# Kernel tuning notes

Measured on AMD Instinct MI355X. Metric: run time of the kernel, lower is better.

The kernel has to match this reference:

```python
import jax, jax.numpy as jnp
import numpy as np

WS = 8  # window_size


def _lstm(x, params):
    """Multi-layer batch-first LSTM with zero initial state (PyTorch gate order i,f,g,o).
    x: [B, Tw, F] -> (outputs [B, Tw, H], (h_n [L,B,H], c_n [L,B,H]))"""
    B = x.shape[0]
    hs_final, cs_final = [], []
    inp = x
    for (Wih, Whh, bih, bhh) in params:
        H = Whh.shape[1]
        b = bih + bhh

        def step(carry, xt, Wih=Wih, Whh=Whh, b=b):
            h, c = carry
            g = xt @ Wih.T + h @ Whh.T + b          # [B, 4H]
            i, f, gg, o = jnp.split(g, 4, axis=-1)
            c = jax.nn.sigmoid(f) * c + jax.nn.sigmoid(i) * jnp.tanh(gg)
            h = jax.nn.sigmoid(o) * jnp.tanh(c)
            return (h, c), h

        h0 = jnp.zeros((B, H), x.dtype)
        (hT, cT), hs = jax.lax.scan(step, (h0, h0), jnp.swapaxes(inp, 0, 1))
        inp = jnp.swapaxes(hs, 0, 1)
        hs_final.append(hT)
        cs_final.append(cT)
    return inp, (jnp.stack(hs_final), jnp.stack(cs_final))


def setup_inputs() -> dict:
    key = jax.random.key(0)
    ks = jax.random.split(key, 11)
    B, T, H, IN = 64, 256, 64, 4
    s = 0.1
    return {
        "traj": jax.random.normal(ks[0], (B, T, IN), jnp.float32),
        "W_ih0": jax.random.normal(ks[1], (4 * H, IN), jnp.float32) * s,
        "W_hh0": jax.random.normal(ks[2], (4 * H, H), jnp.float32) * s,
        "b_ih0": jax.random.normal(ks[3], (4 * H,), jnp.float32) * s,
        "b_hh0": jax.random.normal(ks[4], (4 * H,), jnp.float32) * s,
        "W_ih1": jax.random.normal(ks[5], (4 * H, H), jnp.float32) * s,
        "W_hh1": jax.random.normal(ks[6], (4 * H, H), jnp.float32) * s,
        "b_ih1": jax.random.normal(ks[7], (4 * H,), jnp.float32) * s,
        "b_hh1": jax.random.normal(ks[8], (4 * H,), jnp.float32) * s,
        "W_lin": jax.random.normal(ks[9], (2, H), jnp.float32) * s,
        "b_lin": jax.random.normal(ks[10], (2,), jnp.float32) * s,
    }


def reference(traj, W_ih0, W_hh0, b_ih0, b_hh0, W_ih1, W_hh1, b_ih1, b_hh1, W_lin, b_lin):
    params = [(W_ih0, W_hh0, b_ih0, b_hh0), (W_ih1, W_hh1, b_ih1, b_hh1)]
    lin = lambda x: x @ W_lin.T + b_lin
    B, T = traj.shape[0], traj.shape[1]

    # initial window: teacher-forced, residual update from true state
    lo, hidden = _lstm(traj[:, :WS, :], params)
    out = traj[:, WS - 1:WS, 2:] + lin(lo[:, -1:, :])  # [B, 1, 2]

    # warm-up loop: window mixes remaining true inputs with own predictions
    for t in range(1, WS):
        fb = jnp.concatenate(
            [traj[:, WS + t - 1:WS + t - 1 + out.shape[1], 0:2], out], axis=2)
        x = jnp.concatenate([traj[:, t:WS, :], fb], axis=1)  # [B, WS, 4]
        lo, hidden = _lstm(x, params)
        out = jnp.concatenate([out, out[:, -1:, :] + lin(lo[:, -1:, :])], axis=1)

    # main rollout: each step re-runs the LSTM on a fresh WS-window built from
    # true controls (cols 0:2) and the last WS predictions. Carry a rolling buffer.
    ctrl = traj[:, :, 0:2]

    def step2(carry, t):
        buf, hid = carry  # buf: [B, WS, 2]
        win = jax.lax.dynamic_slice(ctrl, (0, t, 0), (B, WS, 2))
        lo, hid = _lstm(jnp.concatenate([win, buf], axis=2), params)
        new = buf[:, -1:, :] + lin(lo[:, -1:, :])  # [B, 1, 2]
        buf = jnp.concatenate([buf[:, 1:, :], new], axis=1)
        return (buf, hid), new[:, 0, :]

    (buf, hidden), news = jax.lax.scan(step2, (out, hidden), jnp.arange(WS, T - WS))
    out = jnp.concatenate([out, jnp.swapaxes(news, 0, 1)], axis=1)  # [B, T-WS, 2]
    return out, hidden[0], hidden[1]
```

## Files before the change

### kernel.cpp

```cpp
#include <hip/hip_runtime.h>
#include <math.h>

typedef float4 f4;
typedef unsigned long long u64;
#define NW 248
#define NB 64
#define NPH2 (NW + 8)

__device__ __forceinline__ float tanh_f(float x) { return 2.0f * __builtin_amdgcn_rcpf(1.0f + __expf(-2.0f * x)) - 1.0f; }

template<int CTRL>
__device__ __forceinline__ float dppf(float v) {
    return __int_as_float(__builtin_amdgcn_update_dpp(0, __float_as_int(v), CTRL, 0xF, 0xF, true));
}
#define XOR1 0xB1
#define XOR2 0x4E
#define MIR7 0x141
#define BC0  0x00
#define BC1  0x55
#define BC2  0xAA
#define BC3  0xFF

#define OPQ1(X) asm volatile("" : "+v"(X));
#define OPQ4(V) OPQ1(V.x) OPQ1(V.y) OPQ1(V.z) OPQ1(V.w)

#define FMA4(acc,W,H) { acc=fmaf((W).x,(H).x,acc); acc=fmaf((W).y,(H).y,acc); \
                        acc=fmaf((W).z,(H).z,acc); acc=fmaf((W).w,(H).w,acc); }

#define TAIL8(CC, SA, SB, VA, VB, HN)                                                     \
    {                                                                                     \
        float r0=dppf<XOR1>(Q1), r1=dppf<XOR1>(Q0), r2=dppf<XOR1>(Q3), r3=dppf<XOR1>(Q2); \
        float r4=dppf<XOR1>(Q5), r5=dppf<XOR1>(Q4), r6=dppf<XOR1>(Q7), r7=dppf<XOR1>(Q6); \
        Q0+=r0; Q1+=r1; Q2+=r2; Q3+=r3; Q4+=r4; Q5+=r5; Q6+=r6; Q7+=r7;                   \
        float u0=dppf<XOR2>(Q2), u3=dppf<XOR2>(Q1), u4=dppf<XOR2>(Q6), u7=dppf<XOR2>(Q5); \
        Q0+=u0; Q3+=u3; Q4+=u4; Q7+=u7;                                                   \
        float m0=dppf<MIR7>(Q3), m4=dppf<MIR7>(Q7);                                       \
        Q0+=m0; Q4+=m4;                                                                   \
        const float yv = lolane ? Q0 : Q4;                                                \
        const float av = fmaf(fs2, __builtin_amdgcn_rcpf(1.f + __expf(kae*yv)), fs3);     \
        const float gi = dppf<BC0>(av);                                                   \
        const float gf = dppf<BC1>(av);                                                   \
        const float gg = dppf<BC2>(av);                                                   \
        const float go = dppf<BC3>(av);                                                   \
        const bool rst = lolane ? ((SA)==0) : ((SB)==0);                                  \
        const bool upd = lolane ? (VA) : (VB);                                            \
        const float igv = gi * gg;                                                        \
        const float ccn = rst ? igv : fmaf(gf, CC, igv);                                  \
        CC = upd ? ccn : CC;                                                              \
        HN = go * tanh_f(CC);                                                             \
    }

__device__ __forceinline__ float xsel4(float x0, float x1, float x2, float x3, int q2) {
    return (q2 & 2) ? ((q2 & 1) ? x3 : x2) : ((q2 & 1) ? x1 : x0);
}

__device__ __forceinline__ float xload(const float* trajS, const float (*outr)[2],
                                       int w, int s, int q2) {
    float x0, x1, x2, x3;
    if (w == 0) {
        x0 = trajS[s*4+0]; x1 = trajS[s*4+1]; x2 = trajS[s*4+2]; x3 = trajS[s*4+3];
    } else if (w < 8) {
        if (s < 8 - w) {
            const int tt = w + s;
            x0 = trajS[tt*4+0]; x1 = trajS[tt*4+1]; x2 = trajS[tt*4+2]; x3 = trajS[tt*4+3];
        } else {
            const int tc = 2*w + s - 1;
            const int jo2 = (w + s - 8) & 7;
            x0 = trajS[tc*4+0]; x1 = trajS[tc*4+1];
            x2 = outr[jo2][0];  x3 = outr[jo2][1];
        }
    } else {
        const int tc = w + s;
        const int jo2 = (w + s) & 7;
        x0 = trajS[tc*4+0]; x1 = trajS[tc*4+1];
        x2 = outr[jo2][0];  x3 = outr[jo2][1];
    }
    return xsel4(x0, x1, x2, x3, q2);
}

__global__ __launch_bounds__(512) __attribute__((amdgpu_waves_per_eu(2, 2)))
void or_lstm_coop(const float* __restrict__ traj,
                  const float* __restrict__ Wih0, const float* __restrict__ Whh0,
                  const float* __restrict__ bih0, const float* __restrict__ bhh0,
                  const float* __restrict__ Wih1, const float* __restrict__ Whh1,
                  const float* __restrict__ bih1, const float* __restrict__ bhh1,
                  const float* __restrict__ Wlin, const float* __restrict__ blin,
                  float* __restrict__ out, u64* __restrict__ ring)
{
    const int bid  = blockIdx.x;
    const int row  = bid & 63;
    const int half = bid >> 6;
    const int tid  = threadIdx.x;
    const int j    = tid >> 3;
    const int idx  = tid & 7;
    const int q2   = idx & 3;

    __shared__ __align__(16) float trajS[256 * 4];
    __shared__ __align__(16) float X0[2][4][64];
    __shared__ __align__(16) float X1[2][4][64];
    __shared__ float outr[8][2];

    if (tid < 256)
        ((f4*)trajS)[tid] = ((const f4*)(traj + (size_t)row * 256 * 4))[tid];
    ((float*)X0)[tid] = 0.f;
    ((float*)X1)[tid] = 0.f;

    const int jo = j * 64 + idx * 8;
    const int v0 = q2, v1 = 1 ^ q2, v2 = 2 ^ q2, v3 = 3 ^ q2;
    f4 W0a = *(const f4*)(Whh0 + v0*4096 + jo), W0b = *(const f4*)(Whh0 + v0*4096 + jo + 4);
    f4 W1a = *(const f4*)(Whh0 + v1*4096 + jo), W1b = *(const f4*)(Whh0 + v1*4096 + jo + 4);
    f4 W2a = *(const f4*)(Whh0 + v2*4096 + jo), W2b = *(const f4*)(Whh0 + v2*4096 + jo + 4);
    f4 W3a = *(const f4*)(Whh0 + v3*4096 + jo), W3b = *(const f4*)(Whh0 + v3*4096 + jo + 4);
    f4 U0a = *(const f4*)(Wih1 + v0*4096 + jo), U0b = *(const f4*)(Wih1 + v0*4096 + jo + 4);
    f4 U1a = *(const f4*)(Wih1 + v1*4096 + jo), U1b = *(const f4*)(Wih1 + v1*4096 + jo + 4);
    f4 U2a = *(const f4*)(Wih1 + v2*4096 + jo), U2b = *(const f4*)(Wih1 + v2*4096 + jo + 4);
    f4 U3a = *(const f4*)(Wih1 + v3*4096 + jo), U3b = *(const f4*)(Wih1 + v3*4096 + jo + 4);
    f4 V0a = *(const f4*)(Whh1 + v0*4096 + jo), V0b = *(const f4*)(Whh1 + v0*4096 + jo + 4);
    f4 V1a = *(const f4*)(Whh1 + v1*4096 + jo), V1b = *(const f4*)(Whh1 + v1*4096 + jo + 4);
    f4 V2a = *(const f4*)(Whh1 + v2*4096 + jo), V2b = *(const f4*)(Whh1 + v2*4096 + jo + 4);
    f4 V3a = *(const f4*)(Whh1 + v3*4096 + jo), V3b = *(const f4*)(Whh1 + v3*4096 + jo + 4);
    OPQ4(W0a) OPQ4(W0b) OPQ4(W1a) OPQ4(W1b) OPQ4(W2a) OPQ4(W2b) OPQ4(W3a) OPQ4(W3b)
    OPQ4(U0a) OPQ4(U0b) OPQ4(U1a) OPQ4(U1b) OPQ4(U2a) OPQ4(U2b) OPQ4(U3a) OPQ4(U3b)
    OPQ4(V0a) OPQ4(V0b) OPQ4(V1a) OPQ4(V1b) OPQ4(V2a) OPQ4(V2b) OPQ4(V3a) OPQ4(V3b)

    float wx0 = (idx < 4) ? Wih0[v0*256 + j*4 + q2] : 0.f;
    float wx1 = (idx < 4) ? Wih0[v1*256 + j*4 + q2] : 0.f;
    float wx2 = (idx < 4) ? Wih0[v2*256 + j*4 + q2] : 0.f;
    float wx3 = (idx < 4) ? Wih0[v3*256 + j*4 + q2] : 0.f;
    float bb00 = (idx == 0) ? (bih0[0*64+j] + bhh0[0*64+j]) : 0.f;
    float bb01 = (idx == 0) ? (bih0[1*64+j] + bhh0[1*64+j]) : 0.f;
    float bb02 = (idx == 0) ? (bih0[2*64+j] + bhh0[2*64+j]) : 0.f;
    float bb03 = (idx == 0) ? (bih0[3*64+j] + bhh0[3*64+j]) : 0.f;
    float bb10 = (idx == 0) ? (bih1[0*64+j] + bhh1[0*64+j]) : 0.f;
    float bb11 = (idx == 0) ? (bih1[1*64+j] + bhh1[1*64+j]) : 0.f;
    float bb12 = (idx == 0) ? (bih1[2*64+j] + bhh1[2*64+j]) : 0.f;
    float bb13 = (idx == 0) ? (bih1[3*64+j] + bhh1[3*64+j]) : 0.f;
    OPQ1(wx0) OPQ1(wx1) OPQ1(wx2) OPQ1(wx3)
    OPQ1(bb00) OPQ1(bb01) OPQ1(bb02) OPQ1(bb03)
    OPQ1(bb10) OPQ1(bb11) OPQ1(bb12) OPQ1(bb13)

    const float kae = (q2 == 2) ? -2.f : -1.f;
    const float fs2 = (q2 == 2) ?  2.f :  1.f;
    const float fs3 = (q2 == 2) ? -1.f :  0.f;

    float wl0 = 0.f, wl1 = 0.f;
    if (tid < 64) { wl0 = Wlin[tid]; wl1 = Wlin[64 + tid]; }
    const float bl0 = blin[0], bl1 = blin[1];

    const bool lolane = (idx < 4);
    float cc0[2] = {0.f, 0.f};
    float cc1[2] = {0.f, 0.f};

    __syncthreads();

    for (int p = 0; p < NPH2; ++p) {
        const int par = p & 1;
        const float* X0r = &X0[par ^ 1][0][idx * 8];
        const float* X1r = &X1[par ^ 1][0][idx * 8];
        float* X0w = &X0[par][0][j];
        float* X1w = &X1[par][0][j];

        float QM[2][8];

        #pragma unroll
        for (int P = 0; P < 2; ++P) {
            const int cA = 4*half + 2*P, cB = cA + 1;
            const int lA = 2*P,          lB = lA + 1;
            const int sA0 = (p - cA) & 7,     sB0 = (p - cB) & 7;
            const int sA1 = (p - 1 - cA) & 7, sB1 = (p - 1 - cB) & 7;
            const bool vA1 = (unsigned)(p - 1 - sA1) < (unsigned)NW;
            const bool vB1 = (unsigned)(p - 1 - sB1) < (unsigned)NW;

            const f4 ha = *(const f4*)(X0r + lA*64), hb = *(const f4*)(X0r + lA*64 + 4);
            const f4 hc = *(const f4*)(X0r + lB*64), hd = *(const f4*)(X0r + lB*64 + 4);

            {
                float qa0=bb00, qa1=bb01, qa2=bb02, qa3=bb03;
                float qb0=0.f,  qb1=0.f,  qb2=0.f,  qb3=0.f;
                float qa4=bb00, qa5=bb01, qa6=bb02, qa7=bb03;
                float qb4=0.f,  qb5=0.f,  qb6=0.f,  qb7=0.f;
                if (sA0 != 0) {
                    FMA4(qa0, W0a, ha) FMA4(qb0, W0b, hb)
                    FMA4(qa1, W1a, ha) FMA4(qb1, W1b, hb)
                    FMA4(qa2, W2a, ha) FMA4(qb2, W2b, hb)
                    FMA4(qa3, W3a, ha) FMA4(qb3, W3b, hb)
                }
                if (sB0 != 0) {
                    FMA4(qa4, W0a, hc) FMA4(qb4, W0b, hd)
                    FMA4(qa5, W1a, hc) FMA4(qb5, W1b, hd)
                    FMA4(qa6, W2a, hc) FMA4(qb6, W2b, hd)
                    FMA4(qa7, W3a, hc) FMA4(qb7, W3b, hd)
                }
                QM[P][0]=qa0+qb0; QM[P][1]=qa1+qb1; QM[P][2]=qa2+qb2; QM[P][3]=qa3+qb3;
                QM[P][4]=qa4+qb4; QM[P][5]=qa5+qb5; QM[P][6]=qa6+qb6; QM[P][7]=qa7+qb7;
            }

            {
                float pa0=bb10, pa1=bb11, pa2=bb12, pa3=bb13;
                float pb0=0.f,  pb1=0.f,  pb2=0.f,  pb3=0.f;
                float pa4=bb10, pa5=bb11, pa6=bb12, pa7=bb13;
                float pb4=0.f,  pb5=0.f,  pb6=0.f,  pb7=0.f;
                FMA4(pa0, U0a, ha) FMA4(pb0, U0b, hb)
                FMA4(pa1, U1a, ha) FMA4(pb1, U1b, hb)
                FMA4(pa2, U2a, ha) FMA4(pb2, U2b, hb)
                FMA4(pa3, U3a, ha) FMA4(pb3, U3b, hb)
                FMA4(pa4, U0a, hc) FMA4(pb4, U0b, hd)
                FMA4(pa5, U1a, hc) FMA4(pb5, U1b, hd)
                FMA4(pa6, U2a, hc) FMA4(pb6, U2b, hd)
                FMA4(pa7, U3a, hc) FMA4(pb7, U3b, hd)
                if (sA1 != 0) {
                    const f4 ea = *(const f4*)(X1r + lA*64), eb = *(const f4*)(X1r + lA*64 + 4);
                    FMA4(pa0, V0a, ea) FMA4(pb0, V0b, eb)
                    FMA4(pa1, V1a, ea) FMA4(pb1, V1b, eb)
                    FMA4(pa2, V2a, ea) FMA4(pb2, V2b, eb)
                    FMA4(pa3, V3a, ea) FMA4(pb3, V3b, eb)
                }
                if (sB1 != 0) {
                    const f4 ec = *(const f4*)(X1r + lB*64), ed = *(const f4*)(X1r + lB*64 + 4);
                    FMA4(pa4, V0a, ec) FMA4(pb4, V0b, ed)
                    FMA4(pa5, V1a, ec) FMA4(pb5, V1b, ed)
                    FMA4(pa6, V2a, ec) FMA4(pb6, V2b, ed)
                    FMA4(pa7, V3a, ec) FMA4(pb7, V3b, ed)
                }
                float Q0 = pa0+pb0, Q1 = pa1+pb1, Q2 = pa2+pb2, Q3 = pa3+pb3;
                float Q4 = pa4+pb4, Q5 = pa5+pb5, Q6 = pa6+pb6, Q7 = pa7+pb7;
                float hn1;
                TAIL8(cc1[P], sA1, sB1, vA1, vB1, hn1)
                if (vA1 && idx == 0) X1w[lA*64] = hn1;
                if (vB1 && idx == 4) X1w[lB*64] = hn1;
            }
        }
        __syncthreads();

        if (p >= 8) {
            const int w1 = p - 8;
            const int gs = p & 7;
            u64* rp = ring + ((size_t)row * 16 + (p & 15)) * 2;
            const unsigned tag = (unsigned)(p + 1);
            if ((gs >> 2) == half) {
                if (tid < 64) {
                    const float hval = X1[par][gs & 3][tid];
                    float r0 = wl0 * hval, r1 = wl1 * hval;
                    #pragma unroll
                    for (int off = 32; off > 0; off >>= 1) {
                        r0 += __shfl_down(r0, off);
                        r1 += __shfl_down(r1, off);
                    }
                    if (tid == 0) {
                        const float prev0 = w1 ? outr[(w1-1) & 7][0] : trajS[7*4+2];
                        const float prev1 = w1 ? outr[(w1-1) & 7][1] : trajS[7*4+3];
                        const float o0 = prev0 + r0 + bl0;
                        const float o1 = prev1 + r1 + bl1;
                        outr[w1 & 7][0] = o0; outr[w1 & 7][1] = o1;
                        out[((size_t)row * NW + w1) * 2 + 0] = o0;
                        out[((size_t)row * NW + w1) * 2 + 1] = o1;
                        const u64 pk0 = ((u64)tag << 32) | (u64)__float_as_uint(o0);
                        const u64 pk1 = ((u64)tag << 32) | (u64)__float_as_uint(o1);
                        __hip_atomic_store(&rp[0], pk0, __ATOMIC_RELEASE, __HIP_MEMORY_SCOPE_AGENT);
                        __hip_atomic_store(&rp[1], pk1, __ATOMIC_RELEASE, __HIP_MEMORY_SCOPE_AGENT);
                    }
                }
            } else {
                if (tid == 0) {
                    u64 va, vb;
                    do { va = __hip_atomic_load(&rp[0], __ATOMIC_ACQUIRE, __HIP_MEMORY_SCOPE_AGENT);
                    } while ((unsigned)(va >> 32) != tag);
                    do { vb = __hip_atomic_load(&rp[1], __ATOMIC_ACQUIRE, __HIP_MEMORY_SCOPE_AGENT);
                    } while ((unsigned)(vb >> 32) != tag);
                    outr[w1 & 7][0] = __uint_as_float((unsigned)va);
                    outr[w1 & 7][1] = __uint_as_float((unsigned)vb);
                }
            }
        }
        __syncthreads();

        float xs0, xs1, xs2, xs3;
        if (p >= 15) {
            const float xc = xsel4(trajS[p*4+0], trajS[p*4+1],
                                   outr[p & 7][0], outr[p & 7][1], q2);
            xs0 = xs1 = xs2 = xs3 = xc;
        } else {
            float t[4];
            #pragma unroll
            for (int c = 0; c < 4; ++c) {
                const int g = 4*half + c;
                const int s = (p - g) & 7;
                const int w = p - s;
                t[c] = ((unsigned)w < (unsigned)NW) ? xload(trajS, outr, w, s, q2) : 0.f;
            }
            xs0 = t[0]; xs1 = t[1]; xs2 = t[2]; xs3 = t[3];
        }
        #pragma unroll
        for (int P = 0; P < 2; ++P) {
            const int cA = 4*half + 2*P, cB = cA + 1;
            const int lA = 2*P,          lB = lA + 1;
            const int sA0 = (p - cA) & 7, sB0 = (p - cB) & 7;
            const bool vA0 = (unsigned)(p - sA0) < (unsigned)NW;
            const bool vB0 = (unsigned)(p - sB0) < (unsigned)NW;
            const float xA = P ? xs2 : xs0;
            const float xB = P ? xs3 : xs1;
            float Q0 = fmaf(wx0, xA, QM[P][0]);
            float Q1 = fmaf(wx1, xA, QM[P][1]);
            float Q2 = fmaf(wx2, xA, QM[P][2]);
            float Q3 = fmaf(wx3, xA, QM[P][3]);
            float Q4 = fmaf(wx0, xB, QM[P][4]);
            float Q5 = fmaf(wx1, xB, QM[P][5]);
            float Q6 = fmaf(wx2, xB, QM[P][6]);
            float Q7 = fmaf(wx3, xB, QM[P][7]);
            float hn0;
            TAIL8(cc0[P], sA0, sB0, vA0, vB0, hn0)
            if (vA0 && idx == 0) X0w[lA*64] = hn0;
            if (vB0 && idx == 4) X0w[lB*64] = hn0;
        }
        __syncthreads();
    }

    if (half == 1 && idx == 4) {
        float* hn = out + (size_t)NB * NW * 2;
        float* cn = hn + 2 * NB * 64;
        hn[(0 * NB + row) * 64 + j] = X0[0][3][j];
        hn[(1 * NB + row) * 64 + j] = X1[1][3][j];
        cn[(0 * NB + row) * 64 + j] = cc0[1];
        cn[(1 * NB + row) * 64 + j] = cc1[1];
    }
}

extern "C" void kernel_launch(void* const* d_in, const int* in_sizes, int n_in,
                              void* d_out, int out_size, void* d_ws, size_t ws_size,
                              hipStream_t stream) {
    const float* traj = (const float*)d_in[0];
    const float* Wih0 = (const float*)d_in[1];
    const float* Whh0 = (const float*)d_in[2];
    const float* bih0 = (const float*)d_in[3];
    const float* bhh0 = (const float*)d_in[4];
    const float* Wih1 = (const float*)d_in[5];
    const float* Whh1 = (const float*)d_in[6];
    const float* bih1 = (const float*)d_in[7];
    const float* bhh1 = (const float*)d_in[8];
    const float* Wlin = (const float*)d_in[9];
    const float* blin = (const float*)d_in[10];
    float* out = (float*)d_out;

    u64* ring = (u64*)d_ws;
    hipMemsetAsync(d_ws, 0, (size_t)NB * 16 * 2 * sizeof(u64), stream);

    void* kargs[] = { (void*)&traj, (void*)&Wih0, (void*)&Whh0, (void*)&bih0, (void*)&bhh0,
                      (void*)&Wih1, (void*)&Whh1, (void*)&bih1, (void*)&bhh1,
                      (void*)&Wlin, (void*)&blin, (void*)&out, (void*)&ring };
    hipLaunchCooperativeKernel((const void*)or_lstm_coop, dim3(NB * 2), dim3(512),
                               kargs, 0, stream);
}
```

Before: 992.3 us.

## Reorder pair compute around producer step and relax ring atomics

In producer phases, the kernel now computes the layer pair holding the needed hidden state first, syncs, runs the linear head and ring publish, then computes the other pair. This shortens the critical path from hidden state to the cross-block handoff. Consumer blocks spin right after their compute instead of after an extra barrier. Ring stores and loads drop from release/acquire to relaxed ordering. The payload is packed with the tag in one 64-bit word, but the relaxed ordering and the barrier count that now differs between producer and consumer branches add correctness and divergence risk.

```diff
diff --git a/kernel.cpp b/kernel.cpp
--- a/kernel.cpp
+++ b/kernel.cpp
@@ -50,6 +50,97 @@
         HN = go * tanh_f(CC);                                                             \
     }
 
+#define PAIR_A(P)                                                                          \
+    {                                                                                      \
+        const int cA_ = 4*half + 2*(P), cB_ = cA_ + 1;                                     \
+        const int sA0_ = (p - cA_) & 7,     sB0_ = (p - cB_) & 7;                          \
+        const int sA1_ = (p - 1 - cA_) & 7, sB1_ = (p - 1 - cB_) & 7;                      \
+        const bool vA1_ = (unsigned)(p - 1 - sA1_) < (unsigned)NW;                         \
+        const bool vB1_ = (unsigned)(p - 1 - sB1_) < (unsigned)NW;                         \
+        const f4 ha = *(const f4*)(X0r + (P)*128),      hb = *(const f4*)(X0r + (P)*128 + 4);  \
+        const f4 hc = *(const f4*)(X0r + (P)*128 + 64), hd = *(const f4*)(X0r + (P)*128 + 68); \
+        {                         \
+            float qa0=bb00, qa1=bb01, qa2=bb02, qa3=bb03;                                  \
+            float qb0=0.f,  qb1=0.f,  qb2=0.f,  qb3=0.f;                                   \
+            float qa4=bb00, qa5=bb01, qa6=bb02, qa7=bb03;                                  \
+            float qb4=0.f,  qb5=0.f,  qb6=0.f,  qb7=0.f;                                   \
+            if (sA0_ != 0) {                                                               \
+                FMA4(qa0, W0a, ha) FMA4(qb0, W0b, hb)                                      \
+                FMA4(qa1, W1a, ha) FMA4(qb1, W1b, hb)                                      \
+                FMA4(qa2, W2a, ha) FMA4(qb2, W2b, hb)                                      \
+                FMA4(qa3, W3a, ha) FMA4(qb3, W3b, hb)                                      \
+            }                                                                              \
+            if (sB0_ != 0) {                                                               \
+                FMA4(qa4, W0a, hc) FMA4(qb4, W0b, hd)                                      \
+                FMA4(qa5, W1a, hc) FMA4(qb5, W1b, hd)                                      \
+                FMA4(qa6, W2a, hc) FMA4(qb6, W2b, hd)                                      \
+                FMA4(qa7, W3a, hc) FMA4(qb7, W3b, hd)                                      \
+            }                                                                              \
+            QM[P][0]=qa0+qb0; QM[P][1]=qa1+qb1; QM[P][2]=qa2+qb2; QM[P][3]=qa3+qb3;        \
+            QM[P][4]=qa4+qb4; QM[P][5]=qa5+qb5; QM[P][6]=qa6+qb6; QM[P][7]=qa7+qb7;        \
+        }                                                                                  \
+        {                        \
+            float pa0=bb10, pa1=bb11, pa2=bb12, pa3=bb13;                                  \
+            float pb0=0.f,  pb1=0.f,  pb2=0.f,  pb3=0.f;                                   \
+            float pa4=bb10, pa5=bb11, pa6=bb12, pa7=bb13;                                  \
+            float pb4=0.f,  pb5=0.f,  pb6=0.f,  pb7=0.f;                                   \
+            FMA4(pa0, U0a, ha) FMA4(pb0, U0b, hb)                                          \
+            FMA4(pa1, U1a, ha) FMA4(pb1, U1b, hb)                                          \
+            FMA4(pa2, U2a, ha) FMA4(pb2, U2b, hb)                                          \
+            FMA4(pa3, U3a, ha) FMA4(pb3, U3b, hb)                                          \
+            FMA4(pa4, U0a, hc) FMA4(pb4, U0b, hd)                                          \
+            FMA4(pa5, U1a, hc) FMA4(pb5, U1b, hd)                                          \
+            FMA4(pa6, U2a, hc) FMA4(pb6, U2b, hd)                                          \
+            FMA4(pa7, U3a, hc) FMA4(pb7, U3b, hd)                                          \
+            if (sA1_ != 0) {                                                               \
+                const f4 ea = *(const f4*)(X1r + (P)*128), eb = *(const f4*)(X1r + (P)*128 + 4); \
+                FMA4(pa0, V0a, ea) FMA4(pb0, V0b, eb)                                      \
+                FMA4(pa1, V1a, ea) FMA4(pb1, V1b, eb)                                      \
+                FMA4(pa2, V2a, ea) FMA4(pb2, V2b, eb)                                      \
+                FMA4(pa3, V3a, ea) FMA4(pb3, V3b, eb)                                      \
+            }                                                                              \
+            if (sB1_ != 0) {                                                               \
+                const f4 ec = *(const f4*)(X1r + (P)*128 + 64), ed = *(const f4*)(X1r + (P)*128 + 68); \
+                FMA4(pa4, V0a, ec) FMA4(pb4, V0b, ed)                                      \
+                FMA4(pa5, V1a, ec) FMA4(pb5, V1b, ed)                                      \
+                FMA4(pa6, V2a, ec) FMA4(pb6, V2b, ed)                                      \
+                FMA4(pa7, V3a, ec) FMA4(pb7, V3b, ed)                                      \
+            }                                                                              \
+            float Q0 = pa0+pb0, Q1 = pa1+pb1, Q2 = pa2+pb2, Q3 = pa3+pb3;                  \
+            float Q4 = pa4+pb4, Q5 = pa5+pb5, Q6 = pa6+pb6, Q7 = pa7+pb7;                  \
+            float hn1_;                                                                    \
+            TAIL8(cc1[P], sA1_, sB1_, vA1_, vB1_, hn1_)                                    \
+            if (vA1_ && idx == 0) X1w[(2*(P))*64]   = hn1_;                                \
+            if (vB1_ && idx == 4) X1w[(2*(P)+1)*64] = hn1_;                                \
+        }                                                                                  \
+    }
+
+#define PRODUCE()                                                                          \
+    if (tid < 64) {                                                                        \
+        const int w1_ = p - 8;                                                             \
+        const float hval_ = X1[par][gs & 3][tid];                                          \
+        float r0_ = wl0 * hval_, r1_ = wl1 * hval_;                                        \
+        _Pragma("unroll")                                                                  \
+        for (int off_ = 32; off_ > 0; off_ >>= 1) {                                        \
+            r0_ += __shfl_down(r0_, off_);                                                 \
+            r1_ += __shfl_down(r1_, off_);                                                 \
+        }                                                                                  \
+        if (tid == 0) {                                                                    \
+            const float prev0_ = w1_ ? outr[(w1_-1) & 7][0] : trajS[7*4+2];                \
+            const float prev1_ = w1_ ? outr[(w1_-1) & 7][1] : trajS[7*4+3];                \
+            const float o0_ = prev0_ + r0_ + bl0;                                          \
+            const float o1_ = prev1_ + r1_ + bl1;                                          \
+            outr[w1_ & 7][0] = o0_; outr[w1_ & 7][1] = o1_;                                \
+            out[((size_t)row * NW + w1_) * 2 + 0] = o0_;                                   \
+            out[((size_t)row * NW + w1_) * 2 + 1] = o1_;                                   \
+            u64* rp_ = ring + ((size_t)row * 16 + (p & 15)) * 2;                           \
+            const u64 pk0_ = ((u64)(unsigned)(p + 1) << 32) | (u64)__float_as_uint(o0_);   \
+            const u64 pk1_ = ((u64)(unsigned)(p + 1) << 32) | (u64)__float_as_uint(o1_);   \
+            __hip_atomic_store(&rp_[0], pk0_, __ATOMIC_RELAXED, __HIP_MEMORY_SCOPE_AGENT); \
+            __hip_atomic_store(&rp_[1], pk1_, __ATOMIC_RELAXED, __HIP_MEMORY_SCOPE_AGENT); \
+        }                                                                                  \
+    }
+
 __device__ __forceinline__ float xsel4(float x0, float x1, float x2, float x3, int q2) {
     return (q2 & 2) ? ((q2 & 1) ? x3 : x2) : ((q2 & 1) ? x1 : x0);
 }
@@ -160,116 +251,36 @@
         float* X0w = &X0[par][0][j];
         float* X1w = &X1[par][0][j];
 
+        const int gs = p & 7;
+        const bool isProd = (p >= 8) && ((gs >> 2) == half);
+
         float QM[2][8];
 
-        #pragma unroll
-        for (int P = 0; P < 2; ++P) {
-            const int cA = 4*half + 2*P, cB = cA + 1;
-            const int lA = 2*P,          lB = lA + 1;
-            const int sA0 = (p - cA) & 7,     sB0 = (p - cB) & 7;
-            const int sA1 = (p - 1 - cA) & 7, sB1 = (p - 1 - cB) & 7;
-            const bool vA1 = (unsigned)(p - 1 - sA1) < (unsigned)NW;
-            const bool vB1 = (unsigned)(p - 1 - sB1) < (unsigned)NW;
-
-            const f4 ha = *(const f4*)(X0r + lA*64), hb = *(const f4*)(X0r + lA*64 + 4);
-            const f4 hc = *(const f4*)(X0r + lB*64), hd = *(const f4*)(X0r + lB*64 + 4);
-
-            {
-                float qa0=bb00, qa1=bb01, qa2=bb02, qa3=bb03;
-                float qb0=0.f,  qb1=0.f,  qb2=0.f,  qb3=0.f;
-                float qa4=bb00, qa5=bb01, qa6=bb02, qa7=bb03;
-                float qb4=0.f,  qb5=0.f,  qb6=0.f,  qb7=0.f;
-                if (sA0 != 0) {
-                    FMA4(qa0, W0a, ha) FMA4(qb0, W0b, hb)
-                    FMA4(qa1, W1a, ha) FMA4(qb1, W1b, hb)
-                    FMA4(qa2, W2a, ha) FMA4(qb2, W2b, hb)
-                    FMA4(qa3, W3a, ha) FMA4(qb3, W3b, hb)
-                }
-                if (sB0 != 0) {
-                    FMA4(qa4, W0a, hc) FMA4(qb4, W0b, hd)
-                    FMA4(qa5, W1a, hc) FMA4(qb5, W1b, hd)
-                    FMA4(qa6, W2a, hc) FMA4(qb6, W2b, hd)
-                    FMA4(qa7, W3a, hc) FMA4(qb7, W3b, hd)
-                }
-                QM[P][0]=qa0+qb0; QM[P][1]=qa1+qb1; QM[P][2]=qa2+qb2; QM[P][3]=qa3+qb3;
-                QM[P][4]=qa4+qb4; QM[P][5]=qa5+qb5; QM[P][6]=qa6+qb6; QM[P][7]=qa7+qb7;
+        if (isProd) {
+            if (((gs >> 1) & 1) == 1) {
+                PAIR_A(1)
+                __syncthreads();
+                PRODUCE()
+                PAIR_A(0)
+            } else {
+                PAIR_A(0)
+                __syncthreads();
+                PRODUCE()
+                PAIR_A(1)
             }
-
-            {
-                float pa0=bb10, pa1=bb11, pa2=bb12, pa3=bb13;
-                float pb0=0.f,  pb1=0.f,  pb2=0.f,  pb3=0.f;
-                float pa4=bb10, pa5=bb11, pa6=bb12, pa7=bb13;
-                float pb4=0.f,  pb5=0.f,  pb6=0.f,  pb7=0.f;
-                FMA4(pa0, U0a, ha) FMA4(pb0, U0b, hb)
-                FMA4(pa1, U1a, ha) FMA4(pb1, U1b, hb)
-                FMA4(pa2, U2a, ha) FMA4(pb2, U2b, hb)
-                FMA4(pa3, U3a, ha) FMA4(pb3, U3b, hb)
-                FMA4(pa4, U0a, hc) FMA4(pb4, U0b, hd)
-                FMA4(pa5, U1a, hc) FMA4(pb5, U1b, hd)
-                FMA4(pa6, U2a, hc) FMA4(pb6, U2b, hd)
-                FMA4(pa7, U3a, hc) FMA4(pb7, U3b, hd)
-                if (sA1 != 0) {
-                    const f4 ea = *(const f4*)(X1r + lA*64), eb = *(const f4*)(X1r + lA*64 + 4);
-                    FMA4(pa0, V0a, ea) FMA4(pb0, V0b, eb)
-                    FMA4(pa1, V1a, ea) FMA4(pb1, V1b, eb)
-                    FMA4(pa2, V2a, ea) FMA4(pb2, V2b, eb)
-                    FMA4(pa3, V3a, ea) FMA4(pb3, V3b, eb)
-                }
-                if (sB1 != 0) {
-                    const f4 ec = *(const f4*)(X1r + lB*64), ed = *(const f4*)(X1r + lB*64 + 4);
-                    FMA4(pa4, V0a, ec) FMA4(pb4, V0b, ed)
-                    FMA4(pa5, V1a, ec) FMA4(pb5, V1b, ed)
-                    FMA4(pa6, V2a, ec) FMA4(pb6, V2b, ed)
-                    FMA4(pa7, V3a, ec) FMA4(pb7, V3b, ed)
-                }
-                float Q0 = pa0+pb0, Q1 = pa1+pb1, Q2 = pa2+pb2, Q3 = pa3+pb3;
-                float Q4 = pa4+pb4, Q5 = pa5+pb5, Q6 = pa6+pb6, Q7 = pa7+pb7;
-                float hn1;
-                TAIL8(cc1[P], sA1, sB1, vA1, vB1, hn1)
-                if (vA1 && idx == 0) X1w[lA*64] = hn1;
-                if (vB1 && idx == 4) X1w[lB*64] = hn1;
-            }
-        }
-        __syncthreads();
-
-        if (p >= 8) {
-            const int w1 = p - 8;
-            const int gs = p & 7;
-            u64* rp = ring + ((size_t)row * 16 + (p & 15)) * 2;
-            const unsigned tag = (unsigned)(p + 1);
-            if ((gs >> 2) == half) {
-                if (tid < 64) {
-                    const float hval = X1[par][gs & 3][tid];
-                    float r0 = wl0 * hval, r1 = wl1 * hval;
-                    #pragma unroll
-                    for (int off = 32; off > 0; off >>= 1) {
-                        r0 += __shfl_down(r0, off);
-                        r1 += __shfl_down(r1, off);
-                    }
-                    if (tid == 0) {
-                        const float prev0 = w1 ? outr[(w1-1) & 7][0] : trajS[7*4+2];
-                        const float prev1 = w1 ? outr[(w1-1) & 7][1] : trajS[7*4+3];
-                        const float o0 = prev0 + r0 + bl0;
-                        const float o1 = prev1 + r1 + bl1;
-                        outr[w1 & 7][0] = o0; outr[w1 & 7][1] = o1;
-                        out[((size_t)row * NW + w1) * 2 + 0] = o0;
-                        out[((size_t)row * NW + w1) * 2 + 1] = o1;
-                        const u64 pk0 = ((u64)tag << 32) | (u64)__float_as_uint(o0);
-                        const u64 pk1 = ((u64)tag << 32) | (u64)__float_as_uint(o1);
-                        __hip_atomic_store(&rp[0], pk0, __ATOMIC_RELEASE, __HIP_MEMORY_SCOPE_AGENT);
-                        __hip_atomic_store(&rp[1], pk1, __ATOMIC_RELEASE, __HIP_MEMORY_SCOPE_AGENT);
-                    }
-                }
-            } else {
-                if (tid == 0) {
-                    u64 va, vb;
-                    do { va = __hip_atomic_load(&rp[0], __ATOMIC_ACQUIRE, __HIP_MEMORY_SCOPE_AGENT);
-                    } while ((unsigned)(va >> 32) != tag);
-                    do { vb = __hip_atomic_load(&rp[1], __ATOMIC_ACQUIRE, __HIP_MEMORY_SCOPE_AGENT);
-                    } while ((unsigned)(vb >> 32) != tag);
-                    outr[w1 & 7][0] = __uint_as_float((unsigned)va);
-                    outr[w1 & 7][1] = __uint_as_float((unsigned)vb);
-                }
+        } else {
+            PAIR_A(0)
+            PAIR_A(1)
+            if (p >= 8 && tid == 0) {
+                u64* rp = ring + ((size_t)row * 16 + (p & 15)) * 2;
+                const unsigned tag = (unsigned)(p + 1);
+                u64 va, vb;
+                do { va = __hip_atomic_load(&rp[0], __ATOMIC_RELAXED, __HIP_MEMORY_SCOPE_AGENT);
+                } while ((unsigned)(va >> 32) != tag);
+                do { vb = __hip_atomic_load(&rp[1], __ATOMIC_RELAXED, __HIP_MEMORY_SCOPE_AGENT);
+                } while ((unsigned)(vb >> 32) != tag);
+                outr[(p - 8) & 7][0] = __uint_as_float((unsigned)va);
+                outr[(p - 8) & 7][1] = __uint_as_float((unsigned)vb);
             }
         }
         __syncthreads();
```

New measurement: 1.211 ms. 1.22x slower.
